# Optimization experiments

Measured on AMD Instinct MI355X. Metric: run time of the kernel, lower is better.

Reference implementation:

```python
import jax, jax.numpy as jnp
import numpy as np
import math

N_HEADS = 32
N_REP = 4
N_KV = N_HEADS // N_REP
HEAD_DIM = 128
MAX_SEQ = 4096
BATCH = 8
Q_LEN = 1


def setup_inputs() -> dict:
    key = jax.random.key(0)
    ks = jax.random.split(key, 7)
    input_pos = jax.random.randint(ks[0], (Q_LEN,), 0, MAX_SEQ, dtype=jnp.int32)
    q = jax.random.normal(ks[1], (N_HEADS, BATCH, Q_LEN, HEAD_DIM), dtype=jnp.float32)
    k = jax.random.normal(ks[2], (N_KV, BATCH, Q_LEN, HEAD_DIM), dtype=jnp.float32)
    v = jax.random.normal(ks[3], (N_KV, BATCH, Q_LEN, HEAD_DIM), dtype=jnp.float32)
    k_cache = jax.random.normal(ks[4], (N_KV, BATCH, MAX_SEQ, HEAD_DIM), dtype=jnp.float32)
    v_cache = jax.random.normal(ks[5], (N_KV, BATCH, MAX_SEQ, HEAD_DIM), dtype=jnp.float32)
    mask = jax.random.normal(ks[6], (MAX_SEQ, MAX_SEQ), dtype=jnp.float32)
    return {"input_pos": input_pos, "q": q, "k": k, "v": v,
            "k_cache": k_cache, "v_cache": v_cache, "mask": mask}


def reference(input_pos, q, k, v, k_cache, v_cache, mask):
    # KV cache update (index_put_ at positions input_pos along seq axis)
    kc = k_cache.at[:, :, input_pos, :].set(k)   # [G, B, S, D]
    vc = v_cache.at[:, :, input_pos, :].set(v)   # [G, B, S, D]
    scale = 1.0 / math.sqrt(HEAD_DIM)
    # group query heads by kv head: head i uses kv group i // n_rep
    qg = q.reshape(N_KV, N_REP, BATCH, Q_LEN, HEAD_DIM)
    scores = jnp.einsum('grbqd,gbsd->grbqs', qg, kc) * scale
    scores = scores + mask[input_pos]            # [Q, S] broadcast
    probs = jax.nn.softmax(scores, axis=-1)
    out = jnp.einsum('grbqs,gbsd->grbqd', probs, vc)  # [G, R, B, Q, D]
    # torch.cat over heads (i = g*n_rep + r) on last dim -> [B, Q, H*D]
    out = out.transpose(2, 3, 0, 1, 4).reshape(BATCH, Q_LEN, N_HEADS * HEAD_DIM)
    return out
```

## Files before the change

### kernel.cpp

```cpp
#include <hip/hip_runtime.h>
#include <math.h>

#define NKV    8
#define NREP   4
#define NH     32
#define BATCH  8
#define D      128
#define SEQ    4096
#define CHUNKS 32
#define CS     128
#define PSTRIDE 130

__global__ __launch_bounds__(256) void attn_partial(
    const int*   __restrict__ input_pos,
    const float* __restrict__ q,
    const float* __restrict__ knew,
    const float* __restrict__ vnew,
    const float* __restrict__ kcache,
    const float* __restrict__ vcache,
    const float* __restrict__ mask,
    float*       __restrict__ ws)
{
    const int pair = blockIdx.x;
    const int c    = blockIdx.y;
    const int g    = pair >> 3;
    const int b    = pair & 7;
    const int t    = threadIdx.x;
    const int w    = t >> 6;
    const int lane = t & 63;
    const int p8   = lane >> 3;
    const int l8   = lane & 7;
    const int pos  = input_pos[0];

    __shared__ float sc[NREP][CS];
    __shared__ float ml[NREP][2];
    __shared__ float opart[4][NREP][D];

    const float  scale  = 0.08838834764831845f;
    const size_t kvbase = (size_t)(g * BATCH + b) * SEQ * D;
    const float* kbase  = kcache + kvbase;
    const float* vbase  = vcache + kvbase;
    const float* mrow   = mask + (size_t)pos * SEQ;
    const float* knewr  = knew + (size_t)(g * BATCH + b) * D;
    const float* vnewr  = vnew + (size_t)(g * BATCH + b) * D;
    const int    s0     = c * CS;

    float4 qv[NREP][4];
    #pragma unroll
    for (int r = 0; r < NREP; ++r) {
        const float4* qr = (const float4*)(q + ((size_t)(g * NREP + r) * BATCH + b) * D
                                           + l8 * 16);
        #pragma unroll
        for (int j = 0; j < 4; ++j) qv[r][j] = qr[j];
    }

    const int rowbase = w * 32;
    #pragma unroll
    for (int i = 0; i < 4; ++i) {
        const int sl = rowbase + i * 8 + p8;
        const int s  = s0 + sl;
        const float* krow = (s == pos) ? knewr : (kbase + (size_t)s * D);
        const float4* k4  = (const float4*)(krow + l8 * 16);
        float4 kb[4];
        #pragma unroll
        for (int j = 0; j < 4; ++j) kb[j] = k4[j];
        const float mval = mrow[s];

        float acc[NREP] = {0.f, 0.f, 0.f, 0.f};
        #pragma unroll
        for (int r = 0; r < NREP; ++r) {
            #pragma unroll
            for (int j = 0; j < 4; ++j) {
                acc[r] = fmaf(kb[j].x, qv[r][j].x, acc[r]);
                acc[r] = fmaf(kb[j].y, qv[r][j].y, acc[r]);
                acc[r] = fmaf(kb[j].z, qv[r][j].z, acc[r]);
                acc[r] = fmaf(kb[j].w, qv[r][j].w, acc[r]);
            }
        }
        #pragma unroll
        for (int off = 1; off < 8; off <<= 1) {
            #pragma unroll
            for (int r = 0; r < NREP; ++r)
                acc[r] += __shfl_xor(acc[r], off);
        }
        if (l8 == 0) {
            #pragma unroll
            for (int r = 0; r < NREP; ++r)
                sc[r][sl] = acc[r] * scale + mval;
        }
    }
    __syncthreads();

    {
        const int r = w;
        float v0 = sc[r][lane];
        float v1 = sc[r][lane + 64];
        float m  = fmaxf(v0, v1);
        #pragma unroll
        for (int off = 1; off < 64; off <<= 1)
            m = fmaxf(m, __shfl_xor(m, off));
        float e0 = __expf(v0 - m);
        float e1 = __expf(v1 - m);
        sc[r][lane]      = e0;
        sc[r][lane + 64] = e1;
        float l = e0 + e1;
        #pragma unroll
        for (int off = 1; off < 64; off <<= 1)
            l += __shfl_xor(l, off);
        if (lane == 0) { ml[r][0] = m; ml[r][1] = l; }
    }
    __syncthreads();

    const int half = lane >> 5;
    const int l32  = lane & 31;
    float4 oacc[NREP];
    #pragma unroll
    for (int r = 0; r < NREP; ++r) oacc[r] = make_float4(0.f, 0.f, 0.f, 0.f);

    #pragma unroll
    for (int it = 0; it < 16; ++it) {
        int sl = w * 32 + it * 2 + half;
        int s  = s0 + sl;
        const float* vrow = (s == pos) ? vnewr : (vbase + (size_t)s * D);
        float4 vv = *(const float4*)(vrow + l32 * 4);
        #pragma unroll
        for (int r = 0; r < NREP; ++r) {
            float pr = sc[r][sl];
            oacc[r].x = fmaf(pr, vv.x, oacc[r].x);
            oacc[r].y = fmaf(pr, vv.y, oacc[r].y);
            oacc[r].z = fmaf(pr, vv.z, oacc[r].z);
            oacc[r].w = fmaf(pr, vv.w, oacc[r].w);
        }
    }
    #pragma unroll
    for (int r = 0; r < NREP; ++r) {
        oacc[r].x += __shfl_xor(oacc[r].x, 32);
        oacc[r].y += __shfl_xor(oacc[r].y, 32);
        oacc[r].z += __shfl_xor(oacc[r].z, 32);
        oacc[r].w += __shfl_xor(oacc[r].w, 32);
    }
    if (half == 0) {
        #pragma unroll
        for (int r = 0; r < NREP; ++r)
            *(float4*)&opart[w][r][l32 * 4] = oacc[r];
    }
    __syncthreads();

    #pragma unroll
    for (int ii = 0; ii < 2; ++ii) {
        int idx = t + ii * 256;
        int r   = idx >> 7;
        int d   = idx & 127;
        float sum = opart[0][r][d] + opart[1][r][d]
                  + opart[2][r][d] + opart[3][r][d];
        size_t base = (((size_t)pair * CHUNKS + c) * NREP + r) * PSTRIDE;
        ws[base + d] = sum;
        if (d == 0) { ws[base + 128] = ml[r][0]; ws[base + 129] = ml[r][1]; }
    }
}

__global__ __launch_bounds__(128) void attn_reduce(
    const float* __restrict__ ws, float* __restrict__ out)
{
    const int idx  = blockIdx.x;
    const int pair = idx >> 2;
    const int r    = idx & 3;
    const int g    = pair >> 3;
    const int b    = pair & 7;
    const int d    = threadIdx.x;

    float mv[CHUNKS], lv[CHUNKS];
    float M = -INFINITY;
    #pragma unroll
    for (int c = 0; c < CHUNKS; ++c) {
        size_t base = (((size_t)pair * CHUNKS + c) * NREP + r) * PSTRIDE;
        float2 t = *(const float2*)&ws[base + 128];
        mv[c] = t.x; lv[c] = t.y;
        M = fmaxf(M, t.x);
    }
    float acc = 0.f, L = 0.f;
    #pragma unroll
    for (int c = 0; c < CHUNKS; ++c) {
        size_t base = (((size_t)pair * CHUNKS + c) * NREP + r) * PSTRIDE;
        float wgt = __expf(mv[c] - M);
        acc += ws[base + d] * wgt;
        L   += lv[c] * wgt;
    }
    int h = g * NREP + r;
    out[(size_t)b * (NH * D) + h * D + d] = acc / L;
}

__global__ __launch_bounds__(256) void attn_full(
    const int*   __restrict__ input_pos,
    const float* __restrict__ q,
    const float* __restrict__ knew,
    const float* __restrict__ vnew,
    const float* __restrict__ kcache,
    const float* __restrict__ vcache,
    const float* __restrict__ mask,
    float*       __restrict__ out)
{
    const int idx = blockIdx.x;
    const int h   = idx >> 3;
    const int b   = idx & 7;
    const int g   = h >> 2;
    const int t   = threadIdx.x;
    const int wave = t >> 6, lane = t & 63, half = lane >> 5, l32 = lane & 31;
    const int pos = input_pos[0];

    __shared__ float sc[SEQ];
    __shared__ float wred[4];
    __shared__ float oacc[2][D];

    const size_t kvbase = (size_t)(g * BATCH + b) * SEQ * D;
    const float* kbase  = kcache + kvbase;
    const float* vbase  = vcache + kvbase;
    const float* mrow   = mask + (size_t)pos * SEQ;
    const float* knewr  = knew + (size_t)(g * BATCH + b) * D;
    const float* vnewr  = vnew + (size_t)(g * BATCH + b) * D;
    const float  scale  = 0.08838834764831845f;

    float4 qv = ((const float4*)(q + (size_t)(h * BATCH + b) * D))[l32];

    for (int p = 0; p < SEQ / 8; ++p) {
        int s = p * 8 + wave * 2 + half;
        const float4* krow = (s == pos) ? (const float4*)knewr
                                        : (const float4*)(kbase + (size_t)s * D);
        float4 kv = krow[l32];
        float acc = qv.x * kv.x + qv.y * kv.y + qv.z * kv.z + qv.w * kv.w;
        #pragma unroll
        for (int off = 1; off < 32; off <<= 1)
            acc += __shfl_xor(acc, off);
        if (l32 == 0) sc[s] = acc * scale + mrow[s];
    }
    __syncthreads();

    float m = -INFINITY;
    for (int s = t; s < SEQ; s += 256) m = fmaxf(m, sc[s]);
    #pragma unroll
    for (int off = 1; off < 64; off <<= 1) m = fmaxf(m, __shfl_xor(m, off));
    if (lane == 0) wred[wave] = m;
    __syncthreads();
    m = fmaxf(fmaxf(wred[0], wred[1]), fmaxf(wred[2], wred[3]));
    __syncthreads();

    float l = 0.f;
    for (int s = t; s < SEQ; s += 256) { float e = __expf(sc[s] - m); sc[s] = e; l += e; }
    #pragma unroll
    for (int off = 1; off < 64; off <<= 1) l += __shfl_xor(l, off);
    __syncthreads();
    if (lane == 0) wred[wave] = l;
    __syncthreads();
    float L = wred[0] + wred[1] + wred[2] + wred[3];

    {
        int hf = t >> 7, d = t & 127;
        float acc = 0.f;
        for (int s = hf * (SEQ / 2); s < (hf + 1) * (SEQ / 2); ++s) {
            const float* vrow = (s == pos) ? vnewr : (vbase + (size_t)s * D);
            acc += sc[s] * vrow[d];
        }
        oacc[hf][d] = acc;
    }
    __syncthreads();
    if (t < D) out[(size_t)b * (NH * D) + h * D + t] = (oacc[0][t] + oacc[1][t]) / L;
}

extern "C" void kernel_launch(void* const* d_in, const int* in_sizes, int n_in,
                              void* d_out, int out_size, void* d_ws, size_t ws_size,
                              hipStream_t stream) {
    const int*   input_pos = (const int*)  d_in[0];
    const float* q         = (const float*)d_in[1];
    const float* k         = (const float*)d_in[2];
    const float* v         = (const float*)d_in[3];
    const float* kcache    = (const float*)d_in[4];
    const float* vcache    = (const float*)d_in[5];
    const float* mask      = (const float*)d_in[6];
    float* out = (float*)d_out;

    const size_t need = (size_t)64 * CHUNKS * NREP * PSTRIDE * sizeof(float);
    if (ws_size >= need) {
        dim3 g1(64, CHUNKS);
        attn_partial<<<g1, 256, 0, stream>>>(input_pos, q, k, v, kcache, vcache, mask,
                                             (float*)d_ws);
        attn_reduce<<<256, 128, 0, stream>>>((const float*)d_ws, out);
    } else {
        attn_full<<<256, 256, 0, stream>>>(input_pos, q, k, v, kcache, vcache, mask, out);
    }
}
```

Measured before the change: 57.76 us.

## Prefetch all K and V rows into registers before compute in partial attention

Each lane now covers 8 floats instead of 16, with 16 lanes per row. All 8 K rows per thread are loaded up front, and V rows are loaded into 16 register float4s before the softmax phase, so V memory traffic overlaps the softmax reductions. It also adds a launch-bounds minimum of 4 blocks per SM. This raises memory-level parallelism for a bandwidth-bound decode kernel, at the cost of more registers and a wider shuffle reduction.

```diff
diff --git a/kernel.cpp b/kernel.cpp
--- a/kernel.cpp
+++ b/kernel.cpp
@@ -11,7 +11,7 @@
 #define CS     128
 #define PSTRIDE 130
 
-__global__ __launch_bounds__(256) void attn_partial(
+__global__ __launch_bounds__(256, 4) void attn_partial(
     const int*   __restrict__ input_pos,
     const float* __restrict__ q,
     const float* __restrict__ knew,
@@ -28,8 +28,8 @@
     const int t    = threadIdx.x;
     const int w    = t >> 6;
     const int lane = t & 63;
-    const int p8   = lane >> 3;
-    const int l8   = lane & 7;
+    const int p4   = lane >> 4;
+    const int l16  = lane & 15;
     const int pos  = input_pos[0];
 
     __shared__ float sc[NREP][CS];
@@ -44,52 +44,68 @@
     const float* knewr  = knew + (size_t)(g * BATCH + b) * D;
     const float* vnewr  = vnew + (size_t)(g * BATCH + b) * D;
     const int    s0     = c * CS;
-
-    float4 qv[NREP][4];
+    const int    rowbase = w * 32;
+
+    float4 qv[NREP][2];
     #pragma unroll
     for (int r = 0; r < NREP; ++r) {
         const float4* qr = (const float4*)(q + ((size_t)(g * NREP + r) * BATCH + b) * D
-                                           + l8 * 16);
-        #pragma unroll
-        for (int j = 0; j < 4; ++j) qv[r][j] = qr[j];
-    }
-
-    const int rowbase = w * 32;
-    #pragma unroll
-    for (int i = 0; i < 4; ++i) {
-        const int sl = rowbase + i * 8 + p8;
-        const int s  = s0 + sl;
+                                           + l16 * 8);
+        qv[r][0] = qr[0];
+        qv[r][1] = qr[1];
+    }
+
+    float4 kb[8][2];
+    #pragma unroll
+    for (int i = 0; i < 8; ++i) {
+        const int s = s0 + rowbase + i * 4 + p4;
         const float* krow = (s == pos) ? knewr : (kbase + (size_t)s * D);
-        const float4* k4  = (const float4*)(krow + l8 * 16);
-        float4 kb[4];
-        #pragma unroll
-        for (int j = 0; j < 4; ++j) kb[j] = k4[j];
-        const float mval = mrow[s];
-
-        float acc[NREP] = {0.f, 0.f, 0.f, 0.f};
+        const float4* k4  = (const float4*)(krow + l16 * 8);
+        kb[i][0] = k4[0];
+        kb[i][1] = k4[1];
+    }
+
+    #pragma unroll
+    for (int i = 0; i < 8; ++i) {
+        const int sl = rowbase + i * 4 + p4;
+        float acc[NREP];
         #pragma unroll
         for (int r = 0; r < NREP; ++r) {
-            #pragma unroll
-            for (int j = 0; j < 4; ++j) {
-                acc[r] = fmaf(kb[j].x, qv[r][j].x, acc[r]);
-                acc[r] = fmaf(kb[j].y, qv[r][j].y, acc[r]);
-                acc[r] = fmaf(kb[j].z, qv[r][j].z, acc[r]);
-                acc[r] = fmaf(kb[j].w, qv[r][j].w, acc[r]);
-            }
-        }
-        #pragma unroll
-        for (int off = 1; off < 8; off <<= 1) {
+            float a;
+            a = kb[i][0].x * qv[r][0].x;
+            a = fmaf(kb[i][0].y, qv[r][0].y, a);
+            a = fmaf(kb[i][0].z, qv[r][0].z, a);
+            a = fmaf(kb[i][0].w, qv[r][0].w, a);
+            a = fmaf(kb[i][1].x, qv[r][1].x, a);
+            a = fmaf(kb[i][1].y, qv[r][1].y, a);
+            a = fmaf(kb[i][1].z, qv[r][1].z, a);
+            a = fmaf(kb[i][1].w, qv[r][1].w, a);
+            acc[r] = a;
+        }
+        #pragma unroll
+        for (int off = 1; off < 16; off <<= 1) {
             #pragma unroll
             for (int r = 0; r < NREP; ++r)
                 acc[r] += __shfl_xor(acc[r], off);
         }
-        if (l8 == 0) {
+        if (l16 == 0) {
+            const float mval = mrow[s0 + sl];
             #pragma unroll
             for (int r = 0; r < NREP; ++r)
                 sc[r][sl] = acc[r] * scale + mval;
         }
     }
     __syncthreads();
+
+    const int half = lane >> 5;
+    const int l32  = lane & 31;
+    float4 vv[16];
+    #pragma unroll
+    for (int it = 0; it < 16; ++it) {
+        const int s = s0 + rowbase + it * 2 + half;
+        const float* vrow = (s == pos) ? vnewr : (vbase + (size_t)s * D);
+        vv[it] = *(const float4*)(vrow + l32 * 4);
+    }
 
     {
         const int r = w;
@@ -111,25 +127,21 @@
     }
     __syncthreads();
 
-    const int half = lane >> 5;
-    const int l32  = lane & 31;
     float4 oacc[NREP];
     #pragma unroll
     for (int r = 0; r < NREP; ++r) oacc[r] = make_float4(0.f, 0.f, 0.f, 0.f);
 
     #pragma unroll
     for (int it = 0; it < 16; ++it) {
-        int sl = w * 32 + it * 2 + half;
-        int s  = s0 + sl;
-        const float* vrow = (s == pos) ? vnewr : (vbase + (size_t)s * D);
-        float4 vv = *(const float4*)(vrow + l32 * 4);
+        const int sl = rowbase + it * 2 + half;
+        const float4 v4 = vv[it];
         #pragma unroll
         for (int r = 0; r < NREP; ++r) {
-            float pr = sc[r][sl];
-            oacc[r].x = fmaf(pr, vv.x, oacc[r].x);
-            oacc[r].y = fmaf(pr, vv.y, oacc[r].y);
-            oacc[r].z = fmaf(pr, vv.z, oacc[r].z);
-            oacc[r].w = fmaf(pr, vv.w, oacc[r].w);
+            const float pr = sc[r][sl];
+            oacc[r].x = fmaf(pr, v4.x, oacc[r].x);
+            oacc[r].y = fmaf(pr, v4.y, oacc[r].y);
+            oacc[r].z = fmaf(pr, v4.z, oacc[r].z);
+            oacc[r].w = fmaf(pr, v4.w, oacc[r].w);
         }
     }
     #pragma unroll
```

Measured after the change: 51.85 us. -10.2%, faster.

## Software-pipeline K/V loads with inline asm and manual vmcnt waits

Applied to the files above, without the earlier changes.

Replaces the plain K and V cache loads with inline-asm global_load_dwordx4 calls and explicit s_waitcnt vmcnt counts. K rows are now kept four loads in flight and V rows eight deep, and the V prefetch is issued before the softmax so it overlaps that phase. The score lane layout moves from 8 to 16 lanes per row, the mask values are loaded once and shuffled to lanes, and the occupancy hint becomes 4 blocks per SM. The aim is to hide memory latency in this bandwidth-bound decode kernel, at the cost of hand-counted waits that are fragile if the compiler reorders or adds memory operations.

```diff
diff --git a/kernel.cpp b/kernel.cpp
--- a/kernel.cpp
+++ b/kernel.cpp
@@ -11,7 +11,19 @@
 #define CS     128
 #define PSTRIDE 130
 
-__global__ __launch_bounds__(256) void attn_partial(
+__device__ __forceinline__ void gload(float4& d, const float* p) {
+    asm volatile("global_load_dwordx4 %0, %1, off" : "=v"(d) : "v"(p));
+}
+__device__ __forceinline__ void gloadf(float& d, const float* p) {
+    asm volatile("global_load_dword %0, %1, off" : "=v"(d) : "v"(p));
+}
+
+#define VMWAIT(n) do { \
+        asm volatile("s_waitcnt vmcnt(" #n ")" ::: "memory"); \
+        __builtin_amdgcn_sched_barrier(0); \
+    } while (0)
+
+__global__ __launch_bounds__(256, 4) void attn_partial(
     const int*   __restrict__ input_pos,
     const float* __restrict__ q,
     const float* __restrict__ knew,
@@ -28,8 +40,10 @@
     const int t    = threadIdx.x;
     const int w    = t >> 6;
     const int lane = t & 63;
-    const int p8   = lane >> 3;
-    const int l8   = lane & 7;
+    const int p4   = lane >> 4;
+    const int l16  = lane & 15;
+    const int half = lane >> 5;
+    const int l32  = lane & 31;
     const int pos  = input_pos[0];
 
     __shared__ float sc[NREP][CS];
@@ -44,52 +58,86 @@
     const float* knewr  = knew + (size_t)(g * BATCH + b) * D;
     const float* vnewr  = vnew + (size_t)(g * BATCH + b) * D;
     const int    s0     = c * CS;
-
-    float4 qv[NREP][4];
+    const int    rowbase = w * 32;
+
+    float4 qv[NREP][2];
+    float  mreg;
     #pragma unroll
     for (int r = 0; r < NREP; ++r) {
-        const float4* qr = (const float4*)(q + ((size_t)(g * NREP + r) * BATCH + b) * D
-                                           + l8 * 16);
-        #pragma unroll
-        for (int j = 0; j < 4; ++j) qv[r][j] = qr[j];
-    }
-
-    const int rowbase = w * 32;
-    #pragma unroll
-    for (int i = 0; i < 4; ++i) {
-        const int sl = rowbase + i * 8 + p8;
-        const int s  = s0 + sl;
-        const float* krow = (s == pos) ? knewr : (kbase + (size_t)s * D);
-        const float4* k4  = (const float4*)(krow + l8 * 16);
-        float4 kb[4];
-        #pragma unroll
-        for (int j = 0; j < 4; ++j) kb[j] = k4[j];
-        const float mval = mrow[s];
-
-        float acc[NREP] = {0.f, 0.f, 0.f, 0.f};
-        #pragma unroll
-        for (int r = 0; r < NREP; ++r) {
-            #pragma unroll
-            for (int j = 0; j < 4; ++j) {
-                acc[r] = fmaf(kb[j].x, qv[r][j].x, acc[r]);
-                acc[r] = fmaf(kb[j].y, qv[r][j].y, acc[r]);
-                acc[r] = fmaf(kb[j].z, qv[r][j].z, acc[r]);
-                acc[r] = fmaf(kb[j].w, qv[r][j].w, acc[r]);
-            }
-        }
-        #pragma unroll
-        for (int off = 1; off < 8; off <<= 1) {
-            #pragma unroll
-            for (int r = 0; r < NREP; ++r)
-                acc[r] += __shfl_xor(acc[r], off);
-        }
-        if (l8 == 0) {
-            #pragma unroll
-            for (int r = 0; r < NREP; ++r)
-                sc[r][sl] = acc[r] * scale + mval;
-        }
-    }
-    __syncthreads();
+        const float* qr = q + ((size_t)(g * NREP + r) * BATCH + b) * D + l16 * 8;
+        gload(qv[r][0], qr);
+        gload(qv[r][1], qr + 4);
+    }
+    gloadf(mreg, mrow + s0 + rowbase + (lane & 31));
+    VMWAIT(0);
+
+    float mval[8];
+    #pragma unroll
+    for (int i = 0; i < 8; ++i)
+        mval[i] = __shfl(mreg, i * 4 + p4);
+
+    float4 kd[4][2];
+
+#define SC_ISSUE(i) do { \
+        const int s_ = s0 + rowbase + (i) * 4 + p4; \
+        const float* kr_ = ((s_ == pos) ? knewr : (kbase + (size_t)s_ * D)) + l16 * 8; \
+        gload(kd[(i) & 3][0], kr_); \
+        gload(kd[(i) & 3][1], kr_ + 4); \
+    } while (0)
+
+#define SC_CONSUME(i, n) do { \
+        VMWAIT(n); \
+        const float4 k0 = kd[(i) & 3][0], k1 = kd[(i) & 3][1]; \
+        float acc[NREP]; \
+        _Pragma("unroll") \
+        for (int r = 0; r < NREP; ++r) { \
+            float a; \
+            a = k0.x * qv[r][0].x; \
+            a = fmaf(k0.y, qv[r][0].y, a); \
+            a = fmaf(k0.z, qv[r][0].z, a); \
+            a = fmaf(k0.w, qv[r][0].w, a); \
+            a = fmaf(k1.x, qv[r][1].x, a); \
+            a = fmaf(k1.y, qv[r][1].y, a); \
+            a = fmaf(k1.z, qv[r][1].z, a); \
+            a = fmaf(k1.w, qv[r][1].w, a); \
+            acc[r] = a; \
+        } \
+        _Pragma("unroll") \
+        for (int off = 1; off < 16; off <<= 1) { \
+            _Pragma("unroll") \
+            for (int r = 0; r < NREP; ++r) \
+                acc[r] += __shfl_xor(acc[r], off); \
+        } \
+        if (l16 == 0) { \
+            const int sl_ = rowbase + (i) * 4 + p4; \
+            _Pragma("unroll") \
+            for (int r = 0; r < NREP; ++r) \
+                sc[r][sl_] = fmaf(acc[r], scale, mval[(i)]); \
+        } \
+    } while (0)
+
+    SC_ISSUE(0); SC_ISSUE(1); SC_ISSUE(2); SC_ISSUE(3);
+    SC_CONSUME(0, 6); SC_ISSUE(4);
+    SC_CONSUME(1, 6); SC_ISSUE(5);
+    SC_CONSUME(2, 6); SC_ISSUE(6);
+    SC_CONSUME(3, 6); SC_ISSUE(7);
+    SC_CONSUME(4, 6);
+    SC_CONSUME(5, 4);
+    SC_CONSUME(6, 2);
+    SC_CONSUME(7, 0);
+
+    __syncthreads();
+
+    float4 vd[8];
+
+#define PV_ISSUE(it) do { \
+        const int s_ = s0 + rowbase + (it) * 2 + half; \
+        const float* vr_ = ((s_ == pos) ? vnewr : (vbase + (size_t)s_ * D)) + l32 * 4; \
+        gload(vd[(it) & 7], vr_); \
+    } while (0)
+
+    PV_ISSUE(0); PV_ISSUE(1); PV_ISSUE(2); PV_ISSUE(3);
+    PV_ISSUE(4); PV_ISSUE(5); PV_ISSUE(6); PV_ISSUE(7);
 
     {
         const int r = w;
@@ -109,29 +157,45 @@
             l += __shfl_xor(l, off);
         if (lane == 0) { ml[r][0] = m; ml[r][1] = l; }
     }
-    __syncthreads();
-
-    const int half = lane >> 5;
-    const int l32  = lane & 31;
+    asm volatile("s_waitcnt lgkmcnt(0)" ::: "memory");
+    __builtin_amdgcn_sched_barrier(0);
+    __builtin_amdgcn_s_barrier();
+
     float4 oacc[NREP];
     #pragma unroll
     for (int r = 0; r < NREP; ++r) oacc[r] = make_float4(0.f, 0.f, 0.f, 0.f);
 
-    #pragma unroll
-    for (int it = 0; it < 16; ++it) {
-        int sl = w * 32 + it * 2 + half;
-        int s  = s0 + sl;
-        const float* vrow = (s == pos) ? vnewr : (vbase + (size_t)s * D);
-        float4 vv = *(const float4*)(vrow + l32 * 4);
-        #pragma unroll
-        for (int r = 0; r < NREP; ++r) {
-            float pr = sc[r][sl];
-            oacc[r].x = fmaf(pr, vv.x, oacc[r].x);
-            oacc[r].y = fmaf(pr, vv.y, oacc[r].y);
-            oacc[r].z = fmaf(pr, vv.z, oacc[r].z);
-            oacc[r].w = fmaf(pr, vv.w, oacc[r].w);
-        }
-    }
+#define PV_CONSUME(it, n) do { \
+        VMWAIT(n); \
+        const float4 v4 = vd[(it) & 7]; \
+        const int sl_ = rowbase + (it) * 2 + half; \
+        _Pragma("unroll") \
+        for (int r = 0; r < NREP; ++r) { \
+            const float pr = sc[r][sl_]; \
+            oacc[r].x = fmaf(pr, v4.x, oacc[r].x); \
+            oacc[r].y = fmaf(pr, v4.y, oacc[r].y); \
+            oacc[r].z = fmaf(pr, v4.z, oacc[r].z); \
+            oacc[r].w = fmaf(pr, v4.w, oacc[r].w); \
+        } \
+    } while (0)
+
+    PV_CONSUME(0, 7);  PV_ISSUE(8);
+    PV_CONSUME(1, 7);  PV_ISSUE(9);
+    PV_CONSUME(2, 7);  PV_ISSUE(10);
+    PV_CONSUME(3, 7);  PV_ISSUE(11);
+    PV_CONSUME(4, 7);  PV_ISSUE(12);
+    PV_CONSUME(5, 7);  PV_ISSUE(13);
+    PV_CONSUME(6, 7);  PV_ISSUE(14);
+    PV_CONSUME(7, 7);  PV_ISSUE(15);
+    PV_CONSUME(8, 7);
+    PV_CONSUME(9, 6);
+    PV_CONSUME(10, 5);
+    PV_CONSUME(11, 4);
+    PV_CONSUME(12, 3);
+    PV_CONSUME(13, 2);
+    PV_CONSUME(14, 1);
+    PV_CONSUME(15, 0);
+
     #pragma unroll
     for (int r = 0; r < NREP; ++r) {
         oacc[r].x += __shfl_xor(oacc[r].x, 32);
@@ -144,7 +208,9 @@
         for (int r = 0; r < NREP; ++r)
             *(float4*)&opart[w][r][l32 * 4] = oacc[r];
     }
-    __syncthreads();
+    asm volatile("s_waitcnt lgkmcnt(0)" ::: "memory");
+    __builtin_amdgcn_sched_barrier(0);
+    __builtin_amdgcn_s_barrier();
 
     #pragma unroll
     for (int ii = 0; ii < 2; ++ii) {
```

Measured after the change: 53.36 us. 7.6% less time.
